# Optimization experiments

Hardware: AMD Instinct MI355X
Metric: run time of the kernel (lower is better)

## Reference

```python
import jax, jax.numpy as jnp
import numpy as np

EPS = 1e-7  # K.epsilon()
ROUTINGS = 3


def squash(v, axis=-1):
    s2 = jnp.sum(jnp.square(v), axis=axis, keepdims=True)
    scale = s2 / (1.0 + s2) / jnp.sqrt(s2 + EPS)
    return scale * v


def setup_inputs() -> dict:
    key = jax.random.key(0)
    k1, k2 = jax.random.split(key)
    B, I, D, O, K = 64, 2048, 8, 32, 16
    x = jax.random.normal(k1, (B, I, D), dtype=jnp.float32)
    W = jax.random.normal(k2, (I, O, D, K), dtype=jnp.float32) * 0.05
    return {"x": x, "W": W}


def reference(x, W):
    # u_hat[b,o,i,k] = sum_d x[b,i,d] * W[i,o,d,k]
    u_hat = jnp.einsum('bid,iodk->boik', x, W)  # [B, O, I, K]
    B, O, I, _ = u_hat.shape
    b = jnp.zeros((B, O, I), dtype=u_hat.dtype)
    v = None
    for i in range(ROUTINGS):
        c = jax.nn.softmax(b, axis=1)                      # over output capsules
        s = jnp.einsum('boi,boik->bok', c, u_hat)          # weighted sum
        v = squash(s)                                      # [B, O, K]
        if i < ROUTINGS - 1:
            agreement = jnp.einsum('boik,bok->boi', u_hat, v)
            b = b + agreement
    return v
```

## Files before the change

### kernel.cpp

```cpp
#include <hip/hip_runtime.h>


__device__ __forceinline__ float4 f4add(float4 a, float4 b) {
    return make_float4(a.x + b.x, a.y + b.y, a.z + b.z, a.w + b.w);
}
__device__ __forceinline__ int swz(int f4) { return f4 ^ ((f4 >> 3) & 7); }

template<int PASS0>
__global__ __launch_bounds__(512, 4)
void pass_kernel(const float* __restrict__ x,
                 const float* __restrict__ W,
                 const float* __restrict__ vin,
                 float* __restrict__ part)
{
    __shared__ __align__(16) float x_lds[32 * 64];
    __shared__ __align__(16) float red[2][16 * 512];

    const int t  = threadIdx.x;
    const int w  = t >> 6;
    const int l  = t & 63;
    const int o  = l & 31;
    const int kk = l >> 5;
    const int bx = blockIdx.x;
    const int ch = bx & 255;
    const int h  = bx >> 8;
    const int i  = ch * 8 + w;

    const int f4a = swz(o * 4 + kk * 2);
    const int f4b = swz(o * 4 + kk * 2 + 1);
    const int bqf = t >> 8;
    const int j2  = t & 255;
    const int sjf = swz(j2 >> 1) * 4 + (j2 & 1) * 2;

    float Wr[8][8];
    {
        const float* wp = W + (size_t)(i * 32 + o) * 128 + kk * 8;
        #pragma unroll
        for (int d = 0; d < 8; ++d) {
            float4 a = *(const float4*)(wp + d * 16);
            float4 b = *(const float4*)(wp + d * 16 + 4);
            Wr[d][0] = a.x; Wr[d][1] = a.y; Wr[d][2] = a.z; Wr[d][3] = a.w;
            Wr[d][4] = b.x; Wr[d][5] = b.y; Wr[d][6] = b.z; Wr[d][7] = b.w;
        }
        #pragma unroll
        for (int d = 0; d < 8; ++d)
            #pragma unroll
            for (int j = 0; j < 8; ++j)
                asm volatile("" : "+v"(Wr[d][j]));
    }
    {
        const int f  = t * 4;
        const int bl = f >> 6, r = f & 63;
        *(float4*)&x_lds[f] =
            *(const float4*)(x + (size_t)(h * 32 + bl) * 16384 + ch * 64 + r);
    }

    #pragma unroll 2
    for (int g = 0; g < 16; ++g) {
        __syncthreads();

        if (g) {
            const float* rp = red[(g - 1) & 1];
            float2 s = make_float2(0.f, 0.f);
            #pragma unroll
            for (int slot = 0; slot < 8; ++slot) {
                const float2 v = *(const float2*)&rp[(slot * 2 + bqf) * 512 + sjf];
                s.x += v.x; s.y += v.y;
            }
            const int b = h * 32 + (g - 1) * 2 + bqf;
            *(float2*)(part + ((size_t)b * 256 + ch) * 512 + j2 * 2) = s;
        }

        float* rw = red[g & 1];
        #pragma unroll
        for (int bq = 0; bq < 2; ++bq) {
            const int bl = g * 2 + bq;
            float4 va, vb;
            if (!PASS0) {
                const float* vp = vin + (size_t)(h * 32 + bl) * 512 + o * 16 + kk * 8;
                va = *(const float4*)vp;
                vb = *(const float4*)(vp + 4);
            }
            float4 xa = *(const float4*)&x_lds[bl * 64 + w * 8];
            float4 xb = *(const float4*)&x_lds[bl * 64 + w * 8 + 4];
            float xr[8] = {xa.x, xa.y, xa.z, xa.w, xb.x, xb.y, xb.z, xb.w};
            float uh[8];
            #pragma unroll
            for (int j = 0; j < 8; ++j) uh[j] = 0.f;
            #pragma unroll
            for (int d = 0; d < 8; ++d) {
                #pragma unroll
                for (int j = 0; j < 8; ++j)
                    uh[j] = fmaf(xr[d], Wr[d][j], uh[j]);
            }
            float c;
            if (PASS0) {
                c = 0.03125f;
            } else {
                float logit = uh[0] * va.x;
                logit = fmaf(uh[1], va.y, logit);
                logit = fmaf(uh[2], va.z, logit);
                logit = fmaf(uh[3], va.w, logit);
                logit = fmaf(uh[4], vb.x, logit);
                logit = fmaf(uh[5], vb.y, logit);
                logit = fmaf(uh[6], vb.z, logit);
                logit = fmaf(uh[7], vb.w, logit);
                logit += __shfl_xor(logit, 32, 64);
                float ex = __expf(logit);
                float sm = ex;
                #pragma unroll
                for (int off = 16; off >= 1; off >>= 1)
                    sm += __shfl_xor(sm, off, 64);
                c = __fdividef(ex, sm);
            }
            *(float4*)&rw[((w * 2 + bq) * 128 + f4a) * 4] =
                make_float4(c * uh[0], c * uh[1], c * uh[2], c * uh[3]);
            *(float4*)&rw[((w * 2 + bq) * 128 + f4b) * 4] =
                make_float4(c * uh[4], c * uh[5], c * uh[6], c * uh[7]);
        }
    }
    __syncthreads();
    {
        const float* rp = red[1];
        float2 s = make_float2(0.f, 0.f);
        #pragma unroll
        for (int slot = 0; slot < 8; ++slot) {
            const float2 v = *(const float2*)&rp[(slot * 2 + bqf) * 512 + sjf];
            s.x += v.x; s.y += v.y;
        }
        const int b = h * 32 + 15 * 2 + bqf;
        *(float2*)(part + ((size_t)b * 256 + ch) * 512 + j2 * 2) = s;
    }
}

template<int PHASE>
__global__ __launch_bounds__(1024)
void reduce_kernel(const float* __restrict__ part,
                   float* __restrict__ vsum,
                   float* __restrict__ out)
{
    __shared__ __align__(16) float4 sred[64][16];
    __shared__ __align__(16) float4 sredB[16][16];
    const int bx = blockIdx.x;
    const int b  = bx >> 3;
    const int q  = bx & 7;
    const int t  = threadIdx.x;
    const int f  = t & 15;
    const int c0 = t >> 4;

    const float4* p4 =
        (const float4*)(part + ((size_t)b * 256 + c0) * 512 + q * 64) + f;
    float4 s = f4add(f4add(p4[0],          p4[64 * 128]),
                     f4add(p4[128 * 128],  p4[192 * 128]));
    sred[c0][f] = s;
    __syncthreads();

    if (t < 256) {
        const int fr = t & 15, r = t >> 4;
        sredB[r][fr] = f4add(f4add(sred[r][fr],      sred[r + 16][fr]),
                             f4add(sred[r + 32][fr], sred[r + 48][fr]));
    }
    __syncthreads();

    if (t < 64) {
        const float* sB = (const float*)sredB;
        float s1 = 0.f;
        #pragma unroll
        for (int r = 0; r < 16; ++r) s1 += sB[r * 64 + t];
        float sq = s1 * s1;
        #pragma unroll
        for (int off = 8; off >= 1; off >>= 1)
            sq += __shfl_xor(sq, off, 16);
        float v = (sq / (1.f + sq) * rsqrtf(sq + 1e-7f)) * s1;
        const size_t idx = (size_t)b * 512 + q * 64 + t;
        if (PHASE == 2)      out[idx]   = v;
        else if (PHASE == 1) vsum[idx] += v;
        else                 vsum[idx]  = v;
    }
}

extern "C" void kernel_launch(void* const* d_in, const int* in_sizes, int n_in,
                              void* d_out, int out_size, void* d_ws, size_t ws_size,
                              hipStream_t stream)
{
    const float* x = (const float*)d_in[0];
    const float* W = (const float*)d_in[1];
    float* out = (float*)d_out;
    char* ws = (char*)d_ws;

    const size_t partB = (size_t)64 * 256 * 512 * 4;
    const size_t vsumB = (size_t)64 * 512 * 4;
    if (ws_size < partB + vsumB) return;

    float* part = (float*)ws;
    float* vsum = (float*)(ws + partB);

    pass_kernel<1><<<512, 512, 0, stream>>>(x, W, vsum, part);
    reduce_kernel<0><<<512, 1024, 0, stream>>>(part, vsum, out);
    pass_kernel<0><<<512, 512, 0, stream>>>(x, W, vsum, part);
    reduce_kernel<1><<<512, 1024, 0, stream>>>(part, vsum, out);
    pass_kernel<0><<<512, 512, 0, stream>>>(x, W, vsum, part);
    reduce_kernel<2><<<512, 1024, 0, stream>>>(part, vsum, out);
}
```

Before: 191.9 us.

## Store routing partial sums in fp16 and use DPP for softmax reduction

The per-chunk partial sums written to global workspace and staged in LDS are now stored as half precision, which halves the workspace traffic between the pass and reduce kernels and the LDS footprint. The reduce kernel is reorganised to read 16-byte half vectors, with each thread summing two rows instead of four. The softmax denominator shuffle reduction is replaced with DPP row ops plus a ds_swizzle. The cost is fp16 rounding of partial sums, which may hurt accuracy, and the LDS swizzle that avoided bank conflicts is dropped.

```diff
diff --git a/kernel.cpp b/kernel.cpp
--- a/kernel.cpp
+++ b/kernel.cpp
@@ -1,20 +1,25 @@
 #include <hip/hip_runtime.h>
-
-
-__device__ __forceinline__ float4 f4add(float4 a, float4 b) {
-    return make_float4(a.x + b.x, a.y + b.y, a.z + b.z, a.w + b.w);
-}
-__device__ __forceinline__ int swz(int f4) { return f4 ^ ((f4 >> 3) & 7); }
+#include <hip/hip_fp16.h>
+
+
+struct __align__(16) H8 { __half2 a, b, c, d; };
+struct __align__(8)  H4 { __half2 a, b; };
+
+template<int CTRL>
+__device__ __forceinline__ float dppadd(float x) {
+    return x + __int_as_float(__builtin_amdgcn_update_dpp(
+        0, __float_as_int(x), CTRL, 0xF, 0xF, true));
+}
 
 template<int PASS0>
 __global__ __launch_bounds__(512, 4)
 void pass_kernel(const float* __restrict__ x,
                  const float* __restrict__ W,
                  const float* __restrict__ vin,
-                 float* __restrict__ part)
+                 __half* __restrict__ part)
 {
-    __shared__ __align__(16) float x_lds[32 * 64];
-    __shared__ __align__(16) float red[2][16 * 512];
+    __shared__ __align__(16) float  x_lds[32 * 64];
+    __shared__ __align__(16) __half redh[2][16][512];
 
     const int t  = threadIdx.x;
     const int w  = t >> 6;
@@ -26,12 +31,6 @@
     const int h  = bx >> 8;
     const int i  = ch * 8 + w;
 
-    const int f4a = swz(o * 4 + kk * 2);
-    const int f4b = swz(o * 4 + kk * 2 + 1);
-    const int bqf = t >> 8;
-    const int j2  = t & 255;
-    const int sjf = swz(j2 >> 1) * 4 + (j2 & 1) * 2;
-
     float Wr[8][8];
     {
         const float* wp = W + (size_t)(i * 32 + o) * 128 + kk * 8;
@@ -59,19 +58,24 @@
     for (int g = 0; g < 16; ++g) {
         __syncthreads();
 
-        if (g) {
-            const float* rp = red[(g - 1) & 1];
-            float2 s = make_float2(0.f, 0.f);
-            #pragma unroll
-            for (int slot = 0; slot < 8; ++slot) {
-                const float2 v = *(const float2*)&rp[(slot * 2 + bqf) * 512 + sjf];
-                s.x += v.x; s.y += v.y;
+        if (g && t < 256) {
+            const int bqf = t >> 7;
+            const int hx  = (t & 127) * 4;
+            const __half* rp = &redh[(g - 1) & 1][0][0];
+            float a0 = 0.f, a1 = 0.f, a2 = 0.f, a3 = 0.f;
+            #pragma unroll
+            for (int s = 0; s < 8; ++s) {
+                H4 v = *(const H4*)(rp + (s * 2 + bqf) * 512 + hx);
+                float2 f0 = __half22float2(v.a), f1 = __half22float2(v.b);
+                a0 += f0.x; a1 += f0.y; a2 += f1.x; a3 += f1.y;
             }
             const int b = h * 32 + (g - 1) * 2 + bqf;
-            *(float2*)(part + ((size_t)b * 256 + ch) * 512 + j2 * 2) = s;
-        }
-
-        float* rw = red[g & 1];
+            H4 o4;
+            o4.a = __floats2half2_rn(a0, a1);
+            o4.b = __floats2half2_rn(a2, a3);
+            *(H4*)(part + ((size_t)b * 256 + ch) * 512 + hx) = o4;
+        }
+
         #pragma unroll
         for (int bq = 0; bq < 2; ++bq) {
             const int bl = g * 2 + bq;
@@ -108,65 +112,84 @@
                 logit += __shfl_xor(logit, 32, 64);
                 float ex = __expf(logit);
                 float sm = ex;
-                #pragma unroll
-                for (int off = 16; off >= 1; off >>= 1)
-                    sm += __shfl_xor(sm, off, 64);
+                sm = dppadd<0xB1>(sm);
+                sm = dppadd<0x4E>(sm);
+                sm = dppadd<0x124>(sm);
+                sm = dppadd<0x128>(sm);
+                sm += __int_as_float(__builtin_amdgcn_ds_swizzle(
+                          __float_as_int(sm), 0x401F));
                 c = __fdividef(ex, sm);
             }
-            *(float4*)&rw[((w * 2 + bq) * 128 + f4a) * 4] =
-                make_float4(c * uh[0], c * uh[1], c * uh[2], c * uh[3]);
-            *(float4*)&rw[((w * 2 + bq) * 128 + f4b) * 4] =
-                make_float4(c * uh[4], c * uh[5], c * uh[6], c * uh[7]);
+            H8 pk;
+            pk.a = __floats2half2_rn(c * uh[0], c * uh[1]);
+            pk.b = __floats2half2_rn(c * uh[2], c * uh[3]);
+            pk.c = __floats2half2_rn(c * uh[4], c * uh[5]);
+            pk.d = __floats2half2_rn(c * uh[6], c * uh[7]);
+            *(H8*)&redh[g & 1][w * 2 + bq][o * 16 + kk * 8] = pk;
         }
     }
     __syncthreads();
-    {
-        const float* rp = red[1];
-        float2 s = make_float2(0.f, 0.f);
-        #pragma unroll
-        for (int slot = 0; slot < 8; ++slot) {
-            const float2 v = *(const float2*)&rp[(slot * 2 + bqf) * 512 + sjf];
-            s.x += v.x; s.y += v.y;
+    if (t < 256) {
+        const int bqf = t >> 7;
+        const int hx  = (t & 127) * 4;
+        const __half* rp = &redh[1][0][0];
+        float a0 = 0.f, a1 = 0.f, a2 = 0.f, a3 = 0.f;
+        #pragma unroll
+        for (int s = 0; s < 8; ++s) {
+            H4 v = *(const H4*)(rp + (s * 2 + bqf) * 512 + hx);
+            float2 f0 = __half22float2(v.a), f1 = __half22float2(v.b);
+            a0 += f0.x; a1 += f0.y; a2 += f1.x; a3 += f1.y;
         }
         const int b = h * 32 + 15 * 2 + bqf;
-        *(float2*)(part + ((size_t)b * 256 + ch) * 512 + j2 * 2) = s;
+        H4 o4;
+        o4.a = __floats2half2_rn(a0, a1);
+        o4.b = __floats2half2_rn(a2, a3);
+        *(H4*)(part + ((size_t)b * 256 + ch) * 512 + hx) = o4;
     }
 }
 
 template<int PHASE>
 __global__ __launch_bounds__(1024)
-void reduce_kernel(const float* __restrict__ part,
+void reduce_kernel(const __half* __restrict__ part,
                    float* __restrict__ vsum,
                    float* __restrict__ out)
 {
-    __shared__ __align__(16) float4 sred[64][16];
-    __shared__ __align__(16) float4 sredB[16][16];
+    __shared__ __align__(16) float sA[128][64];
+    __shared__ __align__(16) float sB[16][64];
     const int bx = blockIdx.x;
     const int b  = bx >> 3;
     const int q  = bx & 7;
     const int t  = threadIdx.x;
-    const int f  = t & 15;
-    const int c0 = t >> 4;
-
-    const float4* p4 =
-        (const float4*)(part + ((size_t)b * 256 + c0) * 512 + q * 64) + f;
-    float4 s = f4add(f4add(p4[0],          p4[64 * 128]),
-                     f4add(p4[128 * 128],  p4[192 * 128]));
-    sred[c0][f] = s;
+    const int f  = t & 7;
+    const int c0 = t >> 3;
+
+    const __half* p0 = part + ((size_t)b * 256 + c0) * 512 + q * 64 + f * 8;
+    float acc[8] = {0.f, 0.f, 0.f, 0.f, 0.f, 0.f, 0.f, 0.f};
+    #pragma unroll
+    for (int rr = 0; rr < 2; ++rr) {
+        H8 v = *(const H8*)(p0 + (size_t)rr * 128 * 512);
+        float2 f0 = __half22float2(v.a), f1 = __half22float2(v.b),
+               f2 = __half22float2(v.c), f3 = __half22float2(v.d);
+        acc[0] += f0.x; acc[1] += f0.y; acc[2] += f1.x; acc[3] += f1.y;
+        acc[4] += f2.x; acc[5] += f2.y; acc[6] += f3.x; acc[7] += f3.y;
+    }
+    *(float4*)&sA[c0][f * 8]     = make_float4(acc[0], acc[1], acc[2], acc[3]);
+    *(float4*)&sA[c0][f * 8 + 4] = make_float4(acc[4], acc[5], acc[6], acc[7]);
     __syncthreads();
 
-    if (t < 256) {
-        const int fr = t & 15, r = t >> 4;
-        sredB[r][fr] = f4add(f4add(sred[r][fr],      sred[r + 16][fr]),
-                             f4add(sred[r + 32][fr], sred[r + 48][fr]));
+    {
+        const int e = t & 63, r4 = t >> 6;
+        float sb = 0.f;
+        #pragma unroll
+        for (int k2 = 0; k2 < 8; ++k2) sb += sA[r4 + k2 * 16][e];
+        sB[r4][e] = sb;
     }
     __syncthreads();
 
     if (t < 64) {
-        const float* sB = (const float*)sredB;
         float s1 = 0.f;
         #pragma unroll
-        for (int r = 0; r < 16; ++r) s1 += sB[r * 64 + t];
+        for (int r = 0; r < 16; ++r) s1 += sB[r][t];
         float sq = s1 * s1;
         #pragma unroll
         for (int off = 8; off >= 1; off >>= 1)
@@ -188,12 +211,12 @@
     float* out = (float*)d_out;
     char* ws = (char*)d_ws;
 
-    const size_t partB = (size_t)64 * 256 * 512 * 4;
+    const size_t partB = (size_t)64 * 256 * 512 * 2;
     const size_t vsumB = (size_t)64 * 512 * 4;
     if (ws_size < partB + vsumB) return;
 
-    float* part = (float*)ws;
-    float* vsum = (float*)(ws + partB);
+    __half* part = (__half*)ws;
+    float*  vsum = (float*)(ws + partB);
 
     pass_kernel<1><<<512, 512, 0, stream>>>(x, W, vsum, part);
     reduce_kernel<0><<<512, 1024, 0, stream>>>(part, vsum, out);
```

After: 181.3 us. 1.06x faster.
